# Kernel tuning notes

Measured on AMD Instinct MI355X. Metric: run time of the kernel, lower is better.

## Reference

```python
import jax, jax.numpy as jnp
import numpy as np

B, T, C = 4, 2048, 1024
H, D = 16, 64  # num_heads, head_dim
P = 64         # prefix length


def setup_inputs() -> dict:
    key = jax.random.key(0)
    ks = jax.random.split(key, 12)
    s = 1.0 / np.sqrt(C)
    return {
        "x": jax.random.normal(ks[0], (B, T, C), dtype=jnp.float32),
        "attn_mask": jax.random.randint(ks[1], (B, 1, 1, T), 0, 2, dtype=jnp.int32),
        "prefix_k": jax.random.normal(ks[2], (B, H, P, D), dtype=jnp.float32),
        "prefix_v": jax.random.normal(ks[3], (B, H, P, D), dtype=jnp.float32),
        "Wq": jax.random.normal(ks[4], (C, C), dtype=jnp.float32) * s,
        "bq": jnp.zeros((C,), dtype=jnp.float32),
        "Wk": jax.random.normal(ks[5], (C, C), dtype=jnp.float32) * s,
        "bk": jnp.zeros((C,), dtype=jnp.float32),
        "Wv": jax.random.normal(ks[6], (C, C), dtype=jnp.float32) * s,
        "bv": jnp.zeros((C,), dtype=jnp.float32),
        "Wo": jax.random.normal(ks[7], (C, C), dtype=jnp.float32) * s,
        "bo": jnp.zeros((C,), dtype=jnp.float32),
    }


def _heads(y):
    # [B,T,C] -> [B,H,T,D]
    return y.reshape(B, T, H, D).transpose(0, 2, 1, 3)


def reference(x, attn_mask, prefix_k, prefix_v, Wq, bq, Wk, bk, Wv, bv, Wo, bo):
    q = _heads(x @ Wq.T + bq)
    k = _heads(x @ Wk.T + bk)
    v = _heads(x @ Wv.T + bv)
    # concat prefix K/V along key dim -> [B,H,P+T,D]
    k = jnp.concatenate([prefix_k, k], axis=2)
    v = jnp.concatenate([prefix_v, v], axis=2)
    # prefix positions are always visible
    prefix_mask = jnp.ones((B, 1, 1, P), dtype=attn_mask.dtype)
    mask = jnp.concatenate([prefix_mask, attn_mask], axis=-1)  # [B,1,1,P+T]
    scores = jnp.einsum('bhtd,bhsd->bhts', q, k) / jnp.sqrt(jnp.asarray(D, x.dtype))
    scores = jnp.where(mask == 0, -jnp.inf, scores)
    w = jax.nn.softmax(scores, axis=-1)
    o = jnp.einsum('bhts,bhsd->bhtd', w, v)
    o = o.transpose(0, 2, 1, 3).reshape(B, T, C)
    return o @ Wo.T + bo
```

## Files before the change

kernel.cpp:

```cpp
#include <hip/hip_runtime.h>
#include <hip/hip_bf16.h>

typedef __bf16 bf16;
typedef __attribute__((ext_vector_type(8))) __bf16 bf16x8;
typedef __attribute__((ext_vector_type(4))) __bf16 bf16x4;
typedef __attribute__((ext_vector_type(4))) float f32x4;
typedef __attribute__((ext_vector_type(16))) float f32x16;

#define MFMA16(a, b, c) __builtin_amdgcn_mfma_f32_16x16x32_bf16(a, b, c, 0, 0, 0)
#define MFMA32(a, b, c) __builtin_amdgcn_mfma_f32_32x32x16_bf16(a, b, c, 0, 0, 0)

__device__ __forceinline__ void gl_lds16(const void* g, void* l) {
    __builtin_amdgcn_global_load_lds(
        (const __attribute__((address_space(1))) void*)g,
        (__attribute__((address_space(3))) void*)l, 16, 0, 0);
}

#define BARRIER() do { asm volatile("" ::: "memory"); \
    __builtin_amdgcn_s_barrier(); asm volatile("" ::: "memory"); } while (0)

#define QSCALE 0.18033688011f
#define LOGBIAS 24.0f

__device__ __forceinline__ int vsig4(int c) {
    return ((c >> 4) << 4) + (((c >> 3) & 1) << 2) + ((c & 4) ? 8 : 0);
}

__global__ __launch_bounds__(256) void prep(
    const float* __restrict__ x, const float* __restrict__ Wq,
    const float* __restrict__ Wk, const float* __restrict__ Wv,
    const float* __restrict__ Wo, const float* __restrict__ pk,
    const float* __restrict__ pv, const int* __restrict__ mask,
    bf16* __restrict__ xb, bf16* __restrict__ wb,
    bf16* __restrict__ k_ws, bf16* __restrict__ vt_ws,
    int* __restrict__ ridx, int* __restrict__ nkv)
{
    const int blk = blockIdx.x, tid = threadIdx.x;
    if (blk < 4) {
        const int b = blk, lane = tid & 63, wv = tid >> 6;
        const int* mb = mask + b * 2048;
        int loc[8], s = 0;
#pragma unroll
        for (int e = 0; e < 8; ++e) { loc[e] = (mb[tid * 8 + e] != 0); s += loc[e]; }
        int inc = s;
#pragma unroll
        for (int off = 1; off < 64; off <<= 1) {
            int t = __shfl_up(inc, off);
            if (lane >= off) inc += t;
        }
        __shared__ int wt[4];
        if (lane == 63) wt[wv] = inc;
        __syncthreads();
        int wo = 0;
        for (int w = 0; w < wv; ++w) wo += wt[w];
        int excl = wo + inc - s;
#pragma unroll
        for (int e = 0; e < 8; ++e) {
            if (loc[e]) ridx[b * 2048 + excl] = tid * 8 + e;
            excl += loc[e];
        }
        if (tid == 255) nkv[b] = 64 + wo + inc;
    } else if (blk < 260) {
        int i = (blk - 4) * 256 + tid;
        {
            int base = i * 4;
            int bh = base >> 12, rem = base & 4095;
            float4 a = *(const float4*)&pk[base];
            bf16x4 ab;
            ab[0] = (bf16)a.x; ab[1] = (bf16)a.y; ab[2] = (bf16)a.z; ab[3] = (bf16)a.w;
            *(bf16x4*)&k_ws[(size_t)bh * (2112 * 64) + rem] = ab;
        }
        {
            int bh = i >> 10, r = i & 1023;
            int d = r >> 4, sq = (r & 15) * 4;
            bf16x4 vb;
#pragma unroll
            for (int e = 0; e < 4; ++e)
                vb[e] = (bf16)pv[(size_t)bh * 4096 + (sq + e) * 64 + d];
            *(bf16x4*)&vt_ws[((size_t)bh * 64 + d) * 2112 + vsig4(sq)] = vb;
        }
    } else {
        int i8 = (blk - 260) * 256 + tid;
        const float* src; bf16* dst; size_t off;
        if (i8 < 1048576) { src = x; dst = xb; off = (size_t)i8; }
        else {
            int j = i8 - 1048576;
            int sel = j >> 17;
            off = (size_t)(j & 131071);
            src = (sel == 0) ? Wq : (sel == 1) ? Wk : (sel == 2) ? Wv : Wo;
            dst = wb + (size_t)sel * 1048576;
        }
        float4 a = *(const float4*)&src[off * 8];
        float4 c = *(const float4*)&src[off * 8 + 4];
        bf16x8 o;
        o[0] = (bf16)a.x; o[1] = (bf16)a.y; o[2] = (bf16)a.z; o[3] = (bf16)a.w;
        o[4] = (bf16)c.x; o[5] = (bf16)c.y; o[6] = (bf16)c.z; o[7] = (bf16)c.w;
        *(bf16x8*)&dst[off * 8] = o;
    }
}

__device__ __forceinline__ void gemm_8phase_256(
    const bf16* aP0, const bf16* aP1, const bf16* aP2, const bf16* aP3,
    const bf16* bP0, const bf16* bP1, const bf16* bP2, const bf16* bP3,
    bf16* lds, const int tid, f32x4 (&acc)[8][4])
{
    const int wave = tid >> 6, lane = tid & 63;
    const int ln = lane & 15, quad = lane >> 4;
    const int wm = wave >> 2, wn = wave & 3;
    const int so = wave * 512;
    const int aoff = (wm * 128 + ln) * 64;
    const int boff = 16384 + (wn * 64 + ln) * 64;
    const int k0c = ((quad    ) ^ (ln & 7)) << 3;
    const int k1c = ((quad + 4) ^ (ln & 7)) << 3;

#define BUFO(u) (((u) & 1) * 32768)
#define STG_H0(u) { gl_lds16(aP0 + (u)*64, lds + BUFO(u) + so); \
                    gl_lds16(aP1 + (u)*64, lds + BUFO(u) + 4096 + so); }
#define STG_H1(u) { gl_lds16(aP2 + (u)*64, lds + BUFO(u) + 8192 + so); \
                    gl_lds16(aP3 + (u)*64, lds + BUFO(u) + 12288 + so); }
#define STG_H2(u) { gl_lds16(bP0 + (u)*64, lds + BUFO(u) + 16384 + so); \
                    gl_lds16(bP1 + (u)*64, lds + BUFO(u) + 20480 + so); }
#define STG_H3(u) { gl_lds16(bP2 + (u)*64, lds + BUFO(u) + 24576 + so); \
                    gl_lds16(bP3 + (u)*64, lds + BUFO(u) + 28672 + so); }

    STG_H0(0); STG_H1(0); STG_H2(0); STG_H3(0);
    STG_H0(1);
    asm volatile("s_waitcnt vmcnt(2)" ::: "memory");
    BARRIER();

#pragma unroll 2
    for (int t = 0; t < 16; ++t) {
        bf16* cur = lds + ((t & 1) ? 32768 : 0);
        bf16x8 fa[4][2], fb01[2][2], fb23[2][2];

#pragma unroll
        for (int mi = 0; mi < 4; ++mi) {
            fa[mi][0] = *(const bf16x8*)(cur + aoff + mi * 1024 + k0c);
            fa[mi][1] = *(const bf16x8*)(cur + aoff + mi * 1024 + k1c);
        }
#pragma unroll
        for (int ni = 0; ni < 2; ++ni) {
            fb01[ni][0] = *(const bf16x8*)(cur + boff + ni * 1024 + k0c);
            fb01[ni][1] = *(const bf16x8*)(cur + boff + ni * 1024 + k1c);
        }
        if (t < 15) STG_H1(t + 1);
        BARRIER();
        __builtin_amdgcn_s_setprio(1);
#pragma unroll
        for (int mi = 0; mi < 4; ++mi)
#pragma unroll
            for (int ni = 0; ni < 2; ++ni) {
                acc[mi][ni] = MFMA16(fa[mi][0], fb01[ni][0], acc[mi][ni]);
                acc[mi][ni] = MFMA16(fa[mi][1], fb01[ni][1], acc[mi][ni]);
            }
        __builtin_amdgcn_s_setprio(0);
        BARRIER();

#pragma unroll
        for (int ni = 0; ni < 2; ++ni) {
            fb23[ni][0] = *(const bf16x8*)(cur + boff + (2 + ni) * 1024 + k0c);
            fb23[ni][1] = *(const bf16x8*)(cur + boff + (2 + ni) * 1024 + k1c);
        }
        if (t < 15) STG_H2(t + 1);
        BARRIER();
        __builtin_amdgcn_s_setprio(1);
#pragma unroll
        for (int mi = 0; mi < 4; ++mi)
#pragma unroll
            for (int ni = 0; ni < 2; ++ni) {
                acc[mi][2 + ni] = MFMA16(fa[mi][0], fb23[ni][0], acc[mi][2 + ni]);
                acc[mi][2 + ni] = MFMA16(fa[mi][1], fb23[ni][1], acc[mi][2 + ni]);
            }
        __builtin_amdgcn_s_setprio(0);
        BARRIER();

#pragma unroll
        for (int mi = 0; mi < 4; ++mi) {
            fa[mi][0] = *(const bf16x8*)(cur + aoff + (4 + mi) * 1024 + k0c);
            fa[mi][1] = *(const bf16x8*)(cur + aoff + (4 + mi) * 1024 + k1c);
        }
        if (t < 15) STG_H3(t + 1);
        BARRIER();
        __builtin_amdgcn_s_setprio(1);
#pragma unroll
        for (int mi = 0; mi < 4; ++mi)
#pragma unroll
            for (int ni = 0; ni < 2; ++ni) {
                acc[4 + mi][ni] = MFMA16(fa[mi][0], fb01[ni][0], acc[4 + mi][ni]);
                acc[4 + mi][ni] = MFMA16(fa[mi][1], fb01[ni][1], acc[4 + mi][ni]);
            }
        __builtin_amdgcn_s_setprio(0);
        BARRIER();

        if (t < 14) {
            STG_H0(t + 2);
            asm volatile("s_waitcnt vmcnt(2)" ::: "memory");
        } else {
            asm volatile("s_waitcnt vmcnt(0)" ::: "memory");
        }
        BARRIER();
        __builtin_amdgcn_s_setprio(1);
#pragma unroll
        for (int mi = 0; mi < 4; ++mi)
#pragma unroll
            for (int ni = 0; ni < 2; ++ni) {
                acc[4 + mi][2 + ni] = MFMA16(fa[mi][0], fb23[ni][0], acc[4 + mi][2 + ni]);
                acc[4 + mi][2 + ni] = MFMA16(fa[mi][1], fb23[ni][1], acc[4 + mi][2 + ni]);
            }
        __builtin_amdgcn_s_setprio(0);
        BARRIER();
    }
#undef BUFO
#undef STG_H0
#undef STG_H1
#undef STG_H2
#undef STG_H3
}

__global__ __launch_bounds__(512, 2) void proj_gemm(
    const bf16* __restrict__ X, const bf16* __restrict__ Wb,
    const float* __restrict__ bq, const float* __restrict__ bk,
    const float* __restrict__ bv, const int* __restrict__ ridx,
    const int* __restrict__ nkv,
    bf16* __restrict__ q_ws, bf16* __restrict__ k_ws, bf16* __restrict__ vt_ws)
{
    __shared__ bf16 lds[65536];
    const int hw = blockIdx.x;
    const int bx = (hw & 7) * 48 + (hw >> 3);
    const int tid = threadIdx.x;
    const int sr = tid >> 3;
    const int csw = ((tid & 7) ^ (sr & 7)) << 3;

    int kind, m0 = 0, bsel = 0, nvis = 0, mbase = 0, n0;
    const bf16* W;
    const float* bias;
    if (bx < 128) {
        kind = 0; m0 = (bx >> 2) * 256; n0 = (bx & 3) * 256;
        W = Wb; bias = bq;
    } else {
        int u = bx - 128;
        kind = 1 + (u >> 7);
        int r = u & 127;
        bsel = r >> 5;
        int rr = r & 31;
        mbase = (rr >> 2) * 256;
        n0 = (rr & 3) * 256;
        nvis = nkv[bsel] - 64;
        if (mbase >= nvis) return;
        W = Wb + (size_t)kind * 1048576;
        bias = (kind == 1) ? bk : bv;
    }

    const bf16 *a0, *a1, *a2, *a3;
    if (kind == 0) {
        a0 = X + (size_t)(m0 + sr) * 1024 + csw;
        a1 = a0 + (size_t)64 * 1024;
        a2 = a0 + (size_t)128 * 1024;
        a3 = a0 + (size_t)192 * 1024;
    } else {
        const int* rb = ridx + bsel * 2048;
        const int nv1 = nvis - 1;
        int g = mbase + sr;
        int e0 = (g       < nv1) ? g       : nv1;
        int e1 = (g + 64  < nv1) ? g + 64  : nv1;
        int e2 = (g + 128 < nv1) ? g + 128 : nv1;
        int e3 = (g + 192 < nv1) ? g + 192 : nv1;
        const bf16* Xb = X + (size_t)bsel * 2048 * 1024 + csw;
        a0 = Xb + (size_t)rb[e0] * 1024;
        a1 = Xb + (size_t)rb[e1] * 1024;
        a2 = Xb + (size_t)rb[e2] * 1024;
        a3 = Xb + (size_t)rb[e3] * 1024;
    }
    const bf16* b0 = W + (size_t)(n0 + sr) * 1024 + csw;
    const bf16* b1 = b0 + (size_t)64 * 1024;
    const bf16* b2 = b0 + (size_t)128 * 1024;
    const bf16* b3 = b0 + (size_t)192 * 1024;

    const f32x4 z4 = {0.f, 0.f, 0.f, 0.f};
    f32x4 acc[8][4];
#pragma unroll
    for (int i = 0; i < 8; ++i)
#pragma unroll
        for (int j = 0; j < 4; ++j) acc[i][j] = z4;

    gemm_8phase_256(a0, a1, a2, a3, b0, b1, b2, b3, lds, tid, acc);

    const int wave = tid >> 6, lane = tid & 63;
    const int ln = lane & 15, quad = lane >> 4;
    const int wm = wave >> 2, wn = wave & 3;
    if (kind == 0) {
#pragma unroll
        for (int ni = 0; ni < 4; ++ni) {
            const int n = n0 + wn * 64 + ni * 16 + ln;
            const float bb = bias[n];
            const int h = n >> 6, d = n & 63;
#pragma unroll
            for (int mi = 0; mi < 8; ++mi) {
                int m = m0 + wm * 128 + mi * 16 + quad * 4;
                int b = m >> 11, tq = m & 2047;
#pragma unroll
                for (int r = 0; r < 4; ++r)
                    q_ws[((size_t)(b * 16 + h) * 2048 + tq + r) * 64 + d] =
                        (bf16)((acc[mi][ni][r] + bb) * QSCALE);
            }
        }
    } else {
#pragma unroll
        for (int ni = 0; ni < 4; ++ni) {
            const int n = n0 + wn * 64 + ni * 16 + ln;
            const float bb = bias[n];
            const int h = n >> 6, d = n & 63;
            const size_t bh64 = (size_t)(bsel * 16 + h);
#pragma unroll
            for (int mi = 0; mi < 8; ++mi) {
                int ml = mbase + wm * 128 + mi * 16 + quad * 4;
                if (kind == 1) {
#pragma unroll
                    for (int r = 0; r < 4; ++r)
                        if (ml + r < nvis)
                            k_ws[(bh64 * 2112 + 64 + ml + r) * 64 + d] =
                                (bf16)(acc[mi][ni][r] + bb);
                } else {
                    int g0 = 64 + ml;
                    int c0v = g0 & 63;
                    int gcol = (g0 & ~63) + vsig4(c0v);
                    if (ml + 3 < nvis) {
                        bf16x4 pb;
#pragma unroll
                        for (int r = 0; r < 4; ++r) pb[r] = (bf16)(acc[mi][ni][r] + bb);
                        *(bf16x4*)&vt_ws[(bh64 * 64 + d) * 2112 + gcol] = pb;
                    } else {
#pragma unroll
                        for (int r = 0; r < 4; ++r)
                            if (ml + r < nvis)
                                vt_ws[(bh64 * 64 + d) * 2112 + gcol + r] =
                                    (bf16)(acc[mi][ni][r] + bb);
                    }
                }
            }
        }
    }
}

__global__ __launch_bounds__(256, 2) void attn_kernel(
    const bf16* __restrict__ Q, const bf16* __restrict__ K,
    const bf16* __restrict__ VT, const int* __restrict__ nk,
    bf16* __restrict__ O)
{
    __shared__ bf16 smem[128 * 72];
    bf16* Ks = smem;
    bf16* Vt = smem + 64 * 72;
    const int tid = threadIdx.x, wave = tid >> 6, lane = tid & 63;
    const int ln = lane & 31, hh = lane >> 5;
    const int hw = blockIdx.x;
    const int bh = (hw & 7) * 8 + ((hw >> 3) & 7);
    const int qx = hw >> 6;
    const int b = bh >> 4, head = bh & 15;
    const bf16* __restrict__ Kb  = K  + (size_t)bh * (2112 * 64);
    const bf16* __restrict__ Vtb = VT + (size_t)bh * (64 * 2112);
    const int nkeys = nk[b];
    const int send = ((nkeys + 63) >> 6) << 6;
    const int qg = qx * 256 + wave * 64 + ln;

    bf16x8 qf0[4], qf1[4];
#pragma unroll
    for (int kt = 0; kt < 4; ++kt) {
        qf0[kt] = *(const bf16x8*)&Q[((size_t)bh * 2048 + qg) * 64 + kt * 16 + hh * 8];
        qf1[kt] = *(const bf16x8*)&Q[((size_t)bh * 2048 + qg + 32) * 64 + kt * 16 + hh * 8];
    }

    f32x16 m24;
#pragma unroll
    for (int r = 0; r < 16; ++r) m24[r] = -LOGBIAS;

    float l0 = 0.f, l1 = 0.f;
    f32x16 acc00, acc01, acc10, acc11;
#pragma unroll
    for (int r = 0; r < 16; ++r) {
        acc00[r] = 0.f; acc01[r] = 0.f; acc10[r] = 0.f; acc11[r] = 0.f;
    }

    const int ks_s = tid >> 3, ks_c = (tid & 7) * 8;
    const int vd = tid >> 3, vs = (tid & 7) * 8;

    bf16x8 kr0, kr1, vr0, vr1;
    kr0 = *(const bf16x8*)&Kb[(size_t)ks_s * 64 + ks_c];
    kr1 = *(const bf16x8*)&Kb[(size_t)(ks_s + 32) * 64 + ks_c];
    vr0 = *(const bf16x8*)&Vtb[(size_t)vd * 2112 + vs];
    vr1 = *(const bf16x8*)&Vtb[(size_t)(vd + 32) * 2112 + vs];

    for (int s0 = 0; s0 < send; s0 += 64) {
        __syncthreads();
        *(bf16x8*)&Ks[ks_s * 72 + ks_c]        = kr0;
        *(bf16x8*)&Ks[(ks_s + 32) * 72 + ks_c] = kr1;
        *(bf16x8*)&Vt[vd * 72 + vs]            = vr0;
        *(bf16x8*)&Vt[(vd + 32) * 72 + vs]     = vr1;
        __syncthreads();

        if (s0 + 64 < send) {
            const int sn = s0 + 64;
            kr0 = *(const bf16x8*)&Kb[(size_t)(sn + ks_s) * 64 + ks_c];
            kr1 = *(const bf16x8*)&Kb[(size_t)(sn + ks_s + 32) * 64 + ks_c];
            vr0 = *(const bf16x8*)&Vtb[(size_t)vd * 2112 + sn + vs];
            vr1 = *(const bf16x8*)&Vtb[(size_t)(vd + 32) * 2112 + sn + vs];
        }

        f32x16 sc0[2], sc1[2];
#pragma unroll
        for (int ts = 0; ts < 2; ++ts) {
            bf16x8 kf = *(const bf16x8*)&Ks[(ts * 32 + ln) * 72 + hh * 8];
            f32x16 sA = MFMA32(kf, qf0[0], m24);
            f32x16 sB = MFMA32(kf, qf1[0], m24);
#pragma unroll
            for (int kt = 1; kt < 4; ++kt) {
                kf = *(const bf16x8*)&Ks[(ts * 32 + ln) * 72 + kt * 16 + hh * 8];
                sA = MFMA32(kf, qf0[kt], sA);
                sB = MFMA32(kf, qf1[kt], sB);
            }
            sc0[ts] = sA; sc1[ts] = sB;
        }

        float rs0 = 0.f, rs1 = 0.f;
        bf16x8 pf0[4], pf1[4];
        if (s0 + 64 <= nkeys) {
#pragma unroll
            for (int ts = 0; ts < 2; ++ts)
#pragma unroll
                for (int rg = 0; rg < 4; ++rg)
#pragma unroll
                    for (int i = 0; i < 4; ++i) {
                        float p0 = __builtin_amdgcn_exp2f(sc0[ts][rg * 4 + i]);
                        float p1 = __builtin_amdgcn_exp2f(sc1[ts][rg * 4 + i]);
                        rs0 += p0; rs1 += p1;
                        pf0[ts * 2 + (rg >> 1)][(rg & 1) * 4 + i] = (bf16)p0;
                        pf1[ts * 2 + (rg >> 1)][(rg & 1) * 4 + i] = (bf16)p1;
                    }
        } else {
#pragma unroll
            for (int ts = 0; ts < 2; ++ts)
#pragma unroll
                for (int rg = 0; rg < 4; ++rg)
#pragma unroll
                    for (int i = 0; i < 4; ++i) {
                        int key = s0 + ts * 32 + rg * 8 + hh * 4 + i;
                        float add = (key < nkeys) ? 0.f : -1e30f;
                        float p0 = __builtin_amdgcn_exp2f(sc0[ts][rg * 4 + i] + add);
                        float p1 = __builtin_amdgcn_exp2f(sc1[ts][rg * 4 + i] + add);
                        rs0 += p0; rs1 += p1;
                        pf0[ts * 2 + (rg >> 1)][(rg & 1) * 4 + i] = (bf16)p0;
                        pf1[ts * 2 + (rg >> 1)][(rg & 1) * 4 + i] = (bf16)p1;
                    }
        }
        l0 += rs0; l1 += rs1;

#pragma unroll
        for (int st = 0; st < 4; ++st) {
            bf16x8 a0 = *(const bf16x8*)&Vt[ln * 72 + st * 16 + hh * 8];
            acc00 = MFMA32(a0, pf0[st], acc00);
            acc10 = MFMA32(a0, pf1[st], acc10);
            bf16x8 a1 = *(const bf16x8*)&Vt[(32 + ln) * 72 + st * 16 + hh * 8];
            acc01 = MFMA32(a1, pf0[st], acc01);
            acc11 = MFMA32(a1, pf1[st], acc11);
        }
    }

    __syncthreads();
    l0 += __shfl_xor(l0, 32);
    l1 += __shfl_xor(l1, 32);
    const float inv0 = 1.0f / l0, inv1 = 1.0f / l1;
    bf16* scratch = smem + wave * (32 * 72);
    const int orow = lane >> 3, oc = (lane & 7) * 8;
    const int qrow0 = qx * 256 + wave * 64;

#pragma unroll
    for (int rg = 0; rg < 4; ++rg) {
        bf16x4 ob;
#pragma unroll
        for (int i = 0; i < 4; ++i) ob[i] = (bf16)(acc00[rg * 4 + i] * inv0);
        *(bf16x4*)&scratch[ln * 72 + rg * 8 + hh * 4] = ob;
#pragma unroll
        for (int i = 0; i < 4; ++i) ob[i] = (bf16)(acc01[rg * 4 + i] * inv0);
        *(bf16x4*)&scratch[ln * 72 + 32 + rg * 8 + hh * 4] = ob;
    }
    __builtin_amdgcn_s_waitcnt(0xC07F);
    __builtin_amdgcn_sched_barrier(0);
#pragma unroll
    for (int pass = 0; pass < 4; ++pass) {
        int ml = pass * 8 + orow;
        bf16x8 ov = *(const bf16x8*)&scratch[ml * 72 + oc];
        *(bf16x8*)&O[((size_t)b * 2048 + qrow0 + ml) * 1024 + head * 64 + oc] = ov;
    }
    __builtin_amdgcn_s_waitcnt(0xC07F);
    __builtin_amdgcn_sched_barrier(0);

#pragma unroll
    for (int rg = 0; rg < 4; ++rg) {
        bf16x4 ob;
#pragma unroll
        for (int i = 0; i < 4; ++i) ob[i] = (bf16)(acc10[rg * 4 + i] * inv1);
        *(bf16x4*)&scratch[ln * 72 + rg * 8 + hh * 4] = ob;
#pragma unroll
        for (int i = 0; i < 4; ++i) ob[i] = (bf16)(acc11[rg * 4 + i] * inv1);
        *(bf16x4*)&scratch[ln * 72 + 32 + rg * 8 + hh * 4] = ob;
    }
    __builtin_amdgcn_s_waitcnt(0xC07F);
    __builtin_amdgcn_sched_barrier(0);
#pragma unroll
    for (int pass = 0; pass < 4; ++pass) {
        int ml = pass * 8 + orow;
        bf16x8 ov = *(const bf16x8*)&scratch[ml * 72 + oc];
        *(bf16x8*)&O[((size_t)b * 2048 + qrow0 + 32 + ml) * 1024 + head * 64 + oc] = ov;
    }
}

__global__ __launch_bounds__(512, 2) void out_proj_gemm(
    const bf16* __restrict__ A, const bf16* __restrict__ W,
    const float* __restrict__ bias, float* __restrict__ out)
{
    __shared__ bf16 lds[65536];
    const int hw = blockIdx.x;
    const int bx = (hw & 7) * 16 + (hw >> 3);
    const int m0 = (bx >> 2) * 256, n0 = (bx & 3) * 256;
    const int tid = threadIdx.x;
    const int sr = tid >> 3;
    const int csw = ((tid & 7) ^ (sr & 7)) << 3;

    const bf16* a0 = A + (size_t)(m0 + sr) * 1024 + csw;
    const bf16* a1 = a0 + (size_t)64 * 1024;
    const bf16* a2 = a0 + (size_t)128 * 1024;
    const bf16* a3 = a0 + (size_t)192 * 1024;
    const bf16* b0 = W + (size_t)(n0 + sr) * 1024 + csw;
    const bf16* b1 = b0 + (size_t)64 * 1024;
    const bf16* b2 = b0 + (size_t)128 * 1024;
    const bf16* b3 = b0 + (size_t)192 * 1024;

    const f32x4 z4 = {0.f, 0.f, 0.f, 0.f};
    f32x4 acc[8][4];
#pragma unroll
    for (int i = 0; i < 8; ++i)
#pragma unroll
        for (int j = 0; j < 4; ++j) acc[i][j] = z4;

    gemm_8phase_256(a0, a1, a2, a3, b0, b1, b2, b3, lds, tid, acc);

    const int wave = tid >> 6, lane = tid & 63;
    const int ln = lane & 15, quad = lane >> 4;
    const int wm = wave >> 2, wn = wave & 3;
#pragma unroll
    for (int ni = 0; ni < 4; ++ni) {
        const int n = n0 + wn * 64 + ni * 16 + ln;
        const float bb = bias[n];
#pragma unroll
        for (int mi = 0; mi < 8; ++mi) {
            int m = m0 + wm * 128 + mi * 16 + quad * 4;
#pragma unroll
            for (int r = 0; r < 4; ++r)
                out[(size_t)(m + r) * 1024 + n] = acc[mi][ni][r] + bb;
        }
    }
}

extern "C" void kernel_launch(void* const* d_in, const int* in_sizes, int n_in,
                              void* d_out, int out_size, void* d_ws, size_t ws_size,
                              hipStream_t stream)
{
    const float* x    = (const float*)d_in[0];
    const int*   mask = (const int*)d_in[1];
    const float* pk   = (const float*)d_in[2];
    const float* pv   = (const float*)d_in[3];
    const float* Wq   = (const float*)d_in[4];
    const float* bq   = (const float*)d_in[5];
    const float* Wk   = (const float*)d_in[6];
    const float* bk   = (const float*)d_in[7];
    const float* Wv   = (const float*)d_in[8];
    const float* bv   = (const float*)d_in[9];
    const float* Wo   = (const float*)d_in[10];
    const float* bo   = (const float*)d_in[11];
    float* out = (float*)d_out;

    bf16* xb    = (bf16*)d_ws;
    bf16* wb    = xb + (size_t)8388608;
    bf16* q_ws  = wb + (size_t)4194304;
    bf16* k_ws  = q_ws + (size_t)8388608;
    bf16* vt_ws = k_ws + (size_t)8650752;
    int*  ridx  = (int*)(vt_ws + (size_t)8650752);
    int*  nkv   = ridx + 4 * 2048;
    bf16* a_ws  = xb;

    prep<<<dim3(6404), 256, 0, stream>>>(x, Wq, Wk, Wv, Wo, pk, pv, mask,
                                         xb, wb, k_ws, vt_ws, ridx, nkv);
    proj_gemm<<<dim3(384), 512, 0, stream>>>(xb, wb, bq, bk, bv, ridx, nkv,
                                             q_ws, k_ws, vt_ws);
    attn_kernel<<<dim3(512), 256, 0, stream>>>(q_ws, k_ws, vt_ws, nkv, a_ws);
    out_proj_gemm<<<dim3(128), 512, 0, stream>>>(a_ws, wb + (size_t)3 * 1048576,
                                                 bo, out);
}
```

Measured before the change: 257.4 us.

## Restructure GEMM pipeline phases, retile out-projection to 128x128, prioritize attention MFMAs

The 8-phase 256x256 GEMM now splits each wave's rows and columns into low and high halves. It stages the next tile's quarters in an order that lets each phase wait only on the data it needs, which removes several barriers per iteration. The proj_gemm epilogue index mapping is updated to match. The out-projection switches to a new 128x128 tile kernel with 256 threads and 512 blocks, aiming for better occupancy on the small output GEMM. The attention kernel also raises wave priority around its MFMA sections. Fewer barriers raise the risk of LDS races, and smaller tiles reduce data reuse.

```diff
diff --git a/kernel.cpp b/kernel.cpp
--- a/kernel.cpp
+++ b/kernel.cpp
@@ -108,24 +108,25 @@
     const int ln = lane & 15, quad = lane >> 4;
     const int wm = wave >> 2, wn = wave & 3;
     const int so = wave * 512;
-    const int aoff = (wm * 128 + ln) * 64;
-    const int boff = 16384 + (wn * 64 + ln) * 64;
+    const int aLo = (wm * 64 + ln) * 64;
+    const int aHi = (128 + wm * 64 + ln) * 64;
+    const int bLo = 16384 + (wn * 32 + ln) * 64;
+    const int bHi = 16384 + (128 + wn * 32 + ln) * 64;
     const int k0c = ((quad    ) ^ (ln & 7)) << 3;
     const int k1c = ((quad + 4) ^ (ln & 7)) << 3;
 
 #define BUFO(u) (((u) & 1) * 32768)
-#define STG_H0(u) { gl_lds16(aP0 + (u)*64, lds + BUFO(u) + so); \
+#define STG_A0(u) { gl_lds16(aP0 + (u)*64, lds + BUFO(u) + so); \
                     gl_lds16(aP1 + (u)*64, lds + BUFO(u) + 4096 + so); }
-#define STG_H1(u) { gl_lds16(aP2 + (u)*64, lds + BUFO(u) + 8192 + so); \
+#define STG_A1(u) { gl_lds16(aP2 + (u)*64, lds + BUFO(u) + 8192 + so); \
                     gl_lds16(aP3 + (u)*64, lds + BUFO(u) + 12288 + so); }
-#define STG_H2(u) { gl_lds16(bP0 + (u)*64, lds + BUFO(u) + 16384 + so); \
+#define STG_B0(u) { gl_lds16(bP0 + (u)*64, lds + BUFO(u) + 16384 + so); \
                     gl_lds16(bP1 + (u)*64, lds + BUFO(u) + 20480 + so); }
-#define STG_H3(u) { gl_lds16(bP2 + (u)*64, lds + BUFO(u) + 24576 + so); \
+#define STG_B1(u) { gl_lds16(bP2 + (u)*64, lds + BUFO(u) + 24576 + so); \
                     gl_lds16(bP3 + (u)*64, lds + BUFO(u) + 28672 + so); }
 
-    STG_H0(0); STG_H1(0); STG_H2(0); STG_H3(0);
-    STG_H0(1);
-    asm volatile("s_waitcnt vmcnt(2)" ::: "memory");
+    STG_A0(0); STG_B0(0); STG_B1(0); STG_A1(0);
+    asm volatile("s_waitcnt vmcnt(4)" ::: "memory");
     BARRIER();
 
 #pragma unroll 2
@@ -135,15 +136,20 @@
 
 #pragma unroll
         for (int mi = 0; mi < 4; ++mi) {
-            fa[mi][0] = *(const bf16x8*)(cur + aoff + mi * 1024 + k0c);
-            fa[mi][1] = *(const bf16x8*)(cur + aoff + mi * 1024 + k1c);
+            fa[mi][0] = *(const bf16x8*)(cur + aLo + mi * 1024 + k0c);
+            fa[mi][1] = *(const bf16x8*)(cur + aLo + mi * 1024 + k1c);
         }
 #pragma unroll
         for (int ni = 0; ni < 2; ++ni) {
-            fb01[ni][0] = *(const bf16x8*)(cur + boff + ni * 1024 + k0c);
-            fb01[ni][1] = *(const bf16x8*)(cur + boff + ni * 1024 + k1c);
-        }
-        if (t < 15) STG_H1(t + 1);
+            fb01[ni][0] = *(const bf16x8*)(cur + bLo + ni * 1024 + k0c);
+            fb01[ni][1] = *(const bf16x8*)(cur + bLo + ni * 1024 + k1c);
+        }
+        if (t < 15) {
+            STG_A0(t + 1);
+            asm volatile("s_waitcnt vmcnt(4)" ::: "memory");
+        } else {
+            asm volatile("s_waitcnt vmcnt(2)" ::: "memory");
+        }
         BARRIER();
         __builtin_amdgcn_s_setprio(1);
 #pragma unroll
@@ -154,14 +160,18 @@
                 acc[mi][ni] = MFMA16(fa[mi][1], fb01[ni][1], acc[mi][ni]);
             }
         __builtin_amdgcn_s_setprio(0);
-        BARRIER();
 
 #pragma unroll
         for (int ni = 0; ni < 2; ++ni) {
-            fb23[ni][0] = *(const bf16x8*)(cur + boff + (2 + ni) * 1024 + k0c);
-            fb23[ni][1] = *(const bf16x8*)(cur + boff + (2 + ni) * 1024 + k1c);
-        }
-        if (t < 15) STG_H2(t + 1);
+            fb23[ni][0] = *(const bf16x8*)(cur + bHi + ni * 1024 + k0c);
+            fb23[ni][1] = *(const bf16x8*)(cur + bHi + ni * 1024 + k1c);
+        }
+        if (t < 15) {
+            STG_B0(t + 1);
+            asm volatile("s_waitcnt vmcnt(4)" ::: "memory");
+        } else {
+            asm volatile("s_waitcnt vmcnt(0)" ::: "memory");
+        }
         BARRIER();
         __builtin_amdgcn_s_setprio(1);
 #pragma unroll
@@ -172,14 +182,13 @@
                 acc[mi][2 + ni] = MFMA16(fa[mi][1], fb23[ni][1], acc[mi][2 + ni]);
             }
         __builtin_amdgcn_s_setprio(0);
-        BARRIER();
 
 #pragma unroll
         for (int mi = 0; mi < 4; ++mi) {
-            fa[mi][0] = *(const bf16x8*)(cur + aoff + (4 + mi) * 1024 + k0c);
-            fa[mi][1] = *(const bf16x8*)(cur + aoff + (4 + mi) * 1024 + k1c);
-        }
-        if (t < 15) STG_H3(t + 1);
+            fa[mi][0] = *(const bf16x8*)(cur + aHi + mi * 1024 + k0c);
+            fa[mi][1] = *(const bf16x8*)(cur + aHi + mi * 1024 + k1c);
+        }
+        if (t < 15) STG_B1(t + 1);
         BARRIER();
         __builtin_amdgcn_s_setprio(1);
 #pragma unroll
@@ -190,13 +199,10 @@
                 acc[4 + mi][ni] = MFMA16(fa[mi][1], fb01[ni][1], acc[4 + mi][ni]);
             }
         __builtin_amdgcn_s_setprio(0);
-        BARRIER();
-
-        if (t < 14) {
-            STG_H0(t + 2);
-            asm volatile("s_waitcnt vmcnt(2)" ::: "memory");
-        } else {
-            asm volatile("s_waitcnt vmcnt(0)" ::: "memory");
+
+        if (t < 15) {
+            STG_A1(t + 1);
+            asm volatile("s_waitcnt vmcnt(4)" ::: "memory");
         }
         BARRIER();
         __builtin_amdgcn_s_setprio(1);
@@ -208,13 +214,12 @@
                 acc[4 + mi][2 + ni] = MFMA16(fa[mi][1], fb23[ni][1], acc[4 + mi][2 + ni]);
             }
         __builtin_amdgcn_s_setprio(0);
-        BARRIER();
     }
 #undef BUFO
-#undef STG_H0
-#undef STG_H1
-#undef STG_H2
-#undef STG_H3
+#undef STG_A0
+#undef STG_A1
+#undef STG_B0
+#undef STG_B1
 }
 
 __global__ __launch_bounds__(512, 2) void proj_gemm(
@@ -290,36 +295,36 @@
     const int wm = wave >> 2, wn = wave & 3;
     if (kind == 0) {
 #pragma unroll
-        for (int ni = 0; ni < 4; ++ni) {
-            const int n = n0 + wn * 64 + ni * 16 + ln;
+        for (int n4 = 0; n4 < 4; ++n4) {
+            const int n = n0 + (n4 >> 1) * 128 + wn * 32 + (n4 & 1) * 16 + ln;
             const float bb = bias[n];
             const int h = n >> 6, d = n & 63;
 #pragma unroll
-            for (int mi = 0; mi < 8; ++mi) {
-                int m = m0 + wm * 128 + mi * 16 + quad * 4;
+            for (int m8 = 0; m8 < 8; ++m8) {
+                int m = m0 + (m8 >> 2) * 128 + wm * 64 + (m8 & 3) * 16 + quad * 4;
                 int b = m >> 11, tq = m & 2047;
 #pragma unroll
                 for (int r = 0; r < 4; ++r)
                     q_ws[((size_t)(b * 16 + h) * 2048 + tq + r) * 64 + d] =
-                        (bf16)((acc[mi][ni][r] + bb) * QSCALE);
+                        (bf16)((acc[m8][n4][r] + bb) * QSCALE);
             }
         }
     } else {
 #pragma unroll
-        for (int ni = 0; ni < 4; ++ni) {
-            const int n = n0 + wn * 64 + ni * 16 + ln;
+        for (int n4 = 0; n4 < 4; ++n4) {
+            const int n = n0 + (n4 >> 1) * 128 + wn * 32 + (n4 & 1) * 16 + ln;
             const float bb = bias[n];
             const int h = n >> 6, d = n & 63;
             const size_t bh64 = (size_t)(bsel * 16 + h);
 #pragma unroll
-            for (int mi = 0; mi < 8; ++mi) {
-                int ml = mbase + wm * 128 + mi * 16 + quad * 4;
+            for (int m8 = 0; m8 < 8; ++m8) {
+                int ml = mbase + (m8 >> 2) * 128 + wm * 64 + (m8 & 3) * 16 + quad * 4;
                 if (kind == 1) {
 #pragma unroll
                     for (int r = 0; r < 4; ++r)
                         if (ml + r < nvis)
                             k_ws[(bh64 * 2112 + 64 + ml + r) * 64 + d] =
-                                (bf16)(acc[mi][ni][r] + bb);
+                                (bf16)(acc[m8][n4][r] + bb);
                 } else {
                     int g0 = 64 + ml;
                     int c0v = g0 & 63;
@@ -327,17 +332,90 @@
                     if (ml + 3 < nvis) {
                         bf16x4 pb;
 #pragma unroll
-                        for (int r = 0; r < 4; ++r) pb[r] = (bf16)(acc[mi][ni][r] + bb);
+                        for (int r = 0; r < 4; ++r) pb[r] = (bf16)(acc[m8][n4][r] + bb);
                         *(bf16x4*)&vt_ws[(bh64 * 64 + d) * 2112 + gcol] = pb;
                     } else {
 #pragma unroll
                         for (int r = 0; r < 4; ++r)
                             if (ml + r < nvis)
                                 vt_ws[(bh64 * 64 + d) * 2112 + gcol + r] =
-                                    (bf16)(acc[mi][ni][r] + bb);
+                                    (bf16)(acc[m8][n4][r] + bb);
                     }
                 }
             }
+        }
+    }
+}
+
+__device__ __forceinline__ void gemm_tile128(
+    const bf16* a0, const bf16* a1, const bf16* a2, const bf16* a3,
+    const bf16* b0, const bf16* b1, const bf16* b2, const bf16* b3,
+    bf16* lds, const int wave, const int lane, f32x4 (&acc)[4][4])
+{
+    const int ln = lane & 15, quad = lane >> 4;
+    const int wm = wave >> 1, wn = wave & 1;
+    const int soA = wave * 512;
+    const int c0 = (quad * 8) ^ ((ln & 7) << 3);
+    const int c1 = (32 + quad * 8) ^ ((ln & 7) << 3);
+    const int aBase = (wm * 64 + ln) * 64;
+    const int bBase = 8192 + (wn * 64 + ln) * 64;
+
+    gl_lds16(a0, lds + soA);
+    gl_lds16(a1, lds + 2048 + soA);
+    gl_lds16(a2, lds + 4096 + soA);
+    gl_lds16(a3, lds + 6144 + soA);
+    gl_lds16(b0, lds + 8192 + soA);
+    gl_lds16(b1, lds + 10240 + soA);
+    gl_lds16(b2, lds + 12288 + soA);
+    gl_lds16(b3, lds + 14336 + soA);
+    gl_lds16(a0 + 64, lds + 16384 + soA);
+    gl_lds16(a1 + 64, lds + 16384 + 2048 + soA);
+    gl_lds16(a2 + 64, lds + 16384 + 4096 + soA);
+    gl_lds16(a3 + 64, lds + 16384 + 6144 + soA);
+
+#pragma unroll 2
+    for (int t = 0; t < 16; ++t) {
+        bf16* cur = lds + ((t & 1) ? 16384 : 0);
+        bf16* nxt = lds + ((t & 1) ? 0 : 16384);
+
+        if (t < 15) asm volatile("s_waitcnt vmcnt(4)" ::: "memory");
+        else        asm volatile("s_waitcnt vmcnt(0)" ::: "memory");
+        BARRIER();
+
+        bf16x8 fa[4][2], fb[4][2];
+#pragma unroll
+        for (int mi = 0; mi < 4; ++mi) {
+            fa[mi][0] = *(const bf16x8*)(cur + aBase + mi * 1024 + c0);
+            fa[mi][1] = *(const bf16x8*)(cur + aBase + mi * 1024 + c1);
+        }
+#pragma unroll
+        for (int ni = 0; ni < 4; ++ni) {
+            fb[ni][0] = *(const bf16x8*)(cur + bBase + ni * 1024 + c0);
+            fb[ni][1] = *(const bf16x8*)(cur + bBase + ni * 1024 + c1);
+        }
+        if (t < 15) {
+            const int kn = (t + 1) * 64;
+            gl_lds16(b0 + kn, nxt + 8192 + soA);
+            gl_lds16(b1 + kn, nxt + 10240 + soA);
+            gl_lds16(b2 + kn, nxt + 12288 + soA);
+            gl_lds16(b3 + kn, nxt + 14336 + soA);
+        }
+        __builtin_amdgcn_s_setprio(1);
+#pragma unroll
+        for (int mi = 0; mi < 4; ++mi)
+#pragma unroll
+            for (int ni = 0; ni < 4; ++ni) {
+                acc[mi][ni] = MFMA16(fa[mi][0], fb[ni][0], acc[mi][ni]);
+                acc[mi][ni] = MFMA16(fa[mi][1], fb[ni][1], acc[mi][ni]);
+            }
+        __builtin_amdgcn_s_setprio(0);
+        BARRIER();
+        if (t < 14) {
+            const int kn = (t + 2) * 64;
+            gl_lds16(a0 + kn, cur + soA);
+            gl_lds16(a1 + kn, cur + 2048 + soA);
+            gl_lds16(a2 + kn, cur + 4096 + soA);
+            gl_lds16(a3 + kn, cur + 6144 + soA);
         }
     }
 }
@@ -406,6 +484,7 @@
         }
 
         f32x16 sc0[2], sc1[2];
+        __builtin_amdgcn_s_setprio(1);
 #pragma unroll
         for (int ts = 0; ts < 2; ++ts) {
             bf16x8 kf = *(const bf16x8*)&Ks[(ts * 32 + ln) * 72 + hh * 8];
@@ -419,6 +498,7 @@
             }
             sc0[ts] = sA; sc1[ts] = sB;
         }
+        __builtin_amdgcn_s_setprio(0);
 
         float rs0 = 0.f, rs1 = 0.f;
         bf16x8 pf0[4], pf1[4];
@@ -453,6 +533,7 @@
         }
         l0 += rs0; l1 += rs1;
 
+        __builtin_amdgcn_s_setprio(1);
 #pragma unroll
         for (int st = 0; st < 4; ++st) {
             bf16x8 a0 = *(const bf16x8*)&Vt[ln * 72 + st * 16 + hh * 8];
@@ -462,6 +543,7 @@
             acc01 = MFMA32(a1, pf0[st], acc01);
             acc11 = MFMA32(a1, pf1[st], acc11);
         }
+        __builtin_amdgcn_s_setprio(0);
     }
 
     __syncthreads();
@@ -513,46 +595,45 @@
     }
 }
 
-__global__ __launch_bounds__(512, 2) void out_proj_gemm(
+__global__ __launch_bounds__(256, 2) void out_proj_gemm(
     const bf16* __restrict__ A, const bf16* __restrict__ W,
     const float* __restrict__ bias, float* __restrict__ out)
 {
-    __shared__ bf16 lds[65536];
+    __shared__ bf16 lds[32768];
     const int hw = blockIdx.x;
-    const int bx = (hw & 7) * 16 + (hw >> 3);
-    const int m0 = (bx >> 2) * 256, n0 = (bx & 3) * 256;
-    const int tid = threadIdx.x;
+    const int bx = (hw & 7) * 64 + (hw >> 3);
+    const int m0 = (bx >> 3) * 128, n0 = (bx & 7) * 128;
+    const int tid = threadIdx.x, wave = tid >> 6, lane = tid & 63;
     const int sr = tid >> 3;
     const int csw = ((tid & 7) ^ (sr & 7)) << 3;
 
     const bf16* a0 = A + (size_t)(m0 + sr) * 1024 + csw;
-    const bf16* a1 = a0 + (size_t)64 * 1024;
-    const bf16* a2 = a0 + (size_t)128 * 1024;
-    const bf16* a3 = a0 + (size_t)192 * 1024;
+    const bf16* a1 = a0 + (size_t)32 * 1024;
+    const bf16* a2 = a0 + (size_t)64 * 1024;
+    const bf16* a3 = a0 + (size_t)96 * 1024;
     const bf16* b0 = W + (size_t)(n0 + sr) * 1024 + csw;
-    const bf16* b1 = b0 + (size_t)64 * 1024;
-    const bf16* b2 = b0 + (size_t)128 * 1024;
-    const bf16* b3 = b0 + (size_t)192 * 1024;
+    const bf16* b1 = b0 + (size_t)32 * 1024;
+    const bf16* b2 = b0 + (size_t)64 * 1024;
+    const bf16* b3 = b0 + (size_t)96 * 1024;
 
     const f32x4 z4 = {0.f, 0.f, 0.f, 0.f};
-    f32x4 acc[8][4];
-#pragma unroll
-    for (int i = 0; i < 8; ++i)
+    f32x4 acc[4][4];
+#pragma unroll
+    for (int i = 0; i < 4; ++i)
 #pragma unroll
         for (int j = 0; j < 4; ++j) acc[i][j] = z4;
 
-    gemm_8phase_256(a0, a1, a2, a3, b0, b1, b2, b3, lds, tid, acc);
-
-    const int wave = tid >> 6, lane = tid & 63;
+    gemm_tile128(a0, a1, a2, a3, b0, b1, b2, b3, lds, wave, lane, acc);
+
     const int ln = lane & 15, quad = lane >> 4;
-    const int wm = wave >> 2, wn = wave & 3;
+    const int wm = wave >> 1, wn = wave & 1;
 #pragma unroll
     for (int ni = 0; ni < 4; ++ni) {
         const int n = n0 + wn * 64 + ni * 16 + ln;
         const float bb = bias[n];
 #pragma unroll
-        for (int mi = 0; mi < 8; ++mi) {
-            int m = m0 + wm * 128 + mi * 16 + quad * 4;
+        for (int mi = 0; mi < 4; ++mi) {
+            int m = m0 + wm * 64 + mi * 16 + quad * 4;
 #pragma unroll
             for (int r = 0; r < 4; ++r)
                 out[(size_t)(m + r) * 1024 + n] = acc[mi][ni][r] + bb;
@@ -592,6 +673,6 @@
     proj_gemm<<<dim3(384), 512, 0, stream>>>(xb, wb, bq, bk, bv, ridx, nkv,
                                              q_ws, k_ws, vt_ws);
     attn_kernel<<<dim3(512), 256, 0, stream>>>(q_ws, k_ws, vt_ws, nkv, a_ws);
-    out_proj_gemm<<<dim3(128), 512, 0, stream>>>(a_ws, wb + (size_t)3 * 1048576,
+    out_proj_gemm<<<dim3(512), 256, 0, stream>>>(a_ws, wb + (size_t)3 * 1048576,
                                                  bo, out);
 }
```

New measurement: 245.1 us. 1.05x faster.
